# Performance work log

Measured on AMD Instinct MI355X. Metric: run time of the kernel, lower is better.

## Reference

```python
import jax, jax.numpy as jnp
import numpy as np

B, LQ, LK, F = 8, 4096, 4096, 64


def setup_inputs() -> dict:
    key = jax.random.key(0)
    ks = jax.random.split(key, 9)
    s = 1.0 / np.sqrt(F)
    return {
        "query": jax.random.normal(ks[0], (B, LQ, F), dtype=jnp.float32),
        "key": jax.random.normal(ks[1], (B, LK, F), dtype=jnp.float32),
        "value": jax.random.normal(ks[2], (B, LQ, F), dtype=jnp.float32),
        "wq": jax.random.normal(ks[3], (F, F), dtype=jnp.float32) * s,
        "bq": jax.random.normal(ks[4], (F,), dtype=jnp.float32) * 0.01,
        "wk": jax.random.normal(ks[5], (F, F), dtype=jnp.float32) * s,
        "bk": jax.random.normal(ks[6], (F,), dtype=jnp.float32) * 0.01,
        "wv": jax.random.normal(ks[7], (F, F), dtype=jnp.float32) * s,
        "bv": jax.random.normal(ks[8], (F,), dtype=jnp.float32) * 0.01,
    }


def reference(query, key, value, wq, bq, wk, bk, wv, bv):
    # nn.Linear: x @ W.T + b
    q = query @ wq.T + bq          # [B, LQ, F]
    k = key @ wk.T + bk            # [B, LK, F]
    v = value @ wv.T + bv          # [B, LQ, F]
    # scores[b, i, j] = <k_i, q_j>; NO 1/sqrt(d) scaling (faithful to source)
    scores = jnp.einsum('bkf,bqf->bkq', k, q)       # [B, LK, LQ]
    attn = jax.nn.softmax(scores, axis=-1)          # softmax over query positions
    return jnp.einsum('bkq,bqf->bkf', attn, v)      # [B, LK, F]
```

## Files before the change

kernel.cpp:

```cpp
#include <hip/hip_runtime.h>


typedef unsigned short u16;
typedef __attribute__((ext_vector_type(4))) unsigned int u32x4;
typedef __attribute__((ext_vector_type(4))) float f32x4;
typedef __attribute__((ext_vector_type(16))) float f32x16;
typedef __attribute__((ext_vector_type(2))) float f32x2;
typedef __attribute__((ext_vector_type(8))) short s16x8;

#define MFMA32(a, bb, c) __builtin_amdgcn_mfma_f32_32x32x16_bf16((a), (bb), (c), 0, 0, 0)
#define MFMA16(a, bb, c) __builtin_amdgcn_mfma_f32_16x16x32_bf16((a), (bb), (c), 0, 0, 0)

#if __has_builtin(__builtin_amdgcn_exp2f)
#define FEXP2(x) __builtin_amdgcn_exp2f(x)
#else
#define FEXP2(x) exp2f(x)
#endif

__device__ __forceinline__ short f2bf(float x) {
    unsigned u = __builtin_bit_cast(unsigned, x);
    u += 0x7fffu + ((u >> 16) & 1u);
    return (short)(u >> 16);
}
__device__ __forceinline__ float bf2f(short h) {
    unsigned u = ((unsigned)(u16)h) << 16;
    return __builtin_bit_cast(float, u);
}
__device__ __forceinline__ f32x4 zero4() { f32x4 r = {0.f, 0.f, 0.f, 0.f}; return r; }

__device__ __forceinline__ unsigned pktrunc(float lo, float hi) {
#if __has_builtin(__builtin_amdgcn_perm)
    return __builtin_amdgcn_perm(__builtin_bit_cast(unsigned, hi),
                                 __builtin_bit_cast(unsigned, lo), 0x07060302u);
#else
    return (__builtin_bit_cast(unsigned, hi) & 0xffff0000u)
         | (__builtin_bit_cast(unsigned, lo) >> 16);
#endif
}

__device__ __forceinline__ void split8(f32x4 a, f32x4 b, s16x8& hi, s16x8& lo) {
#pragma unroll
    for (int i = 0; i < 4; i++) {
        short h = f2bf(a[i]);
        hi[i] = h;
        lo[i] = f2bf(a[i] - bf2f(h));
    }
#pragma unroll
    for (int i = 0; i < 4; i++) {
        short h = f2bf(b[i]);
        hi[i + 4] = h;
        lo[i + 4] = f2bf(b[i] - bf2f(h));
    }
}

__global__ __launch_bounds__(256) void proj_qkv_32727650796335(
    const float* __restrict__ q_, const float* __restrict__ k_, const float* __restrict__ v_,
    const float* __restrict__ wq, const float* __restrict__ bq,
    const float* __restrict__ wk, const float* __restrict__ bk,
    const float* __restrict__ wv, const float* __restrict__ bv,
    u16* __restrict__ qp, u16* __restrict__ kph, u16* __restrict__ kpl,
    u16* __restrict__ vp) {
    const int z = blockIdx.y;
    const float* X  = (z == 0) ? q_ : (z == 1) ? k_ : v_;
    const float* W  = (z == 0) ? wq : (z == 1) ? wk : wv;
    const float* bi = (z == 0) ? bq : (z == 1) ? bk : bv;

    const int t = threadIdx.x;
    const int w = t >> 6, ln = t & 63, g = ln >> 4, lq = ln & 15;
    const int cidx = blockIdx.x;

    __shared__ f32x4 ldsX[1024];
    __shared__ __align__(16) u16 outH[4096];
    __shared__ __align__(16) u16 outLo[4096];

    const f32x4* X4 = (const f32x4*)X + (size_t)cidx * 1024;
#pragma unroll
    for (int kk = 0; kk < 4; kk++) {
        int lin = t + 256 * kk;
        int r = lin >> 4, c4 = lin & 15;
        ldsX[r * 16 + (c4 ^ (r & 7))] = X4[lin];
    }
    __syncthreads();

    float bv4[4];
#pragma unroll
    for (int nt = 0; nt < 4; nt++) bv4[nt] = bi[lq + 16 * nt];

    const f32x4* W4 = (const f32x4*)W;
    s16x8 wfh[4][2], wfl[4][2];
#pragma unroll
    for (int nt = 0; nt < 4; nt++)
#pragma unroll
        for (int kb = 0; kb < 2; kb++) {
            f32x4 a = W4[(lq + 16 * nt) * 16 + (g + 8 * kb)];
            f32x4 b = W4[(lq + 16 * nt) * 16 + (g + 4 + 8 * kb)];
            split8(a, b, wfh[nt][kb], wfl[nt][kb]);
        }

    s16x8 afh[2], afl[2];
#pragma unroll
    for (int kb = 0; kb < 2; kb++) {
        f32x4 a = ldsX[(16 * w + lq) * 16 + ((g + 8 * kb) ^ (lq & 7))];
        f32x4 b = ldsX[(16 * w + lq) * 16 + ((g + 4 + 8 * kb) ^ (lq & 7))];
        split8(a, b, afh[kb], afl[kb]);
    }

    f32x4 acc[4];
#pragma unroll
    for (int nt = 0; nt < 4; nt++) acc[nt] = zero4();
#pragma unroll
    for (int kb = 0; kb < 2; kb++)
#pragma unroll
        for (int nt = 0; nt < 4; nt++) {
            acc[nt] = MFMA16(afh[kb], wfh[nt][kb], acc[nt]);
            acc[nt] = MFMA16(afh[kb], wfl[nt][kb], acc[nt]);
            acc[nt] = MFMA16(afl[kb], wfh[nt][kb], acc[nt]);
        }

#pragma unroll
    for (int nt = 0; nt < 4; nt++)
#pragma unroll
        for (int r = 0; r < 4; r++) {
            float val = acc[nt][r] + bv4[nt];
            if (z == 1) val *= 1.44269504f;
            short hi = f2bf(val);
            int row = 16 * w + 4 * g + r;
            int f = lq + 16 * nt;
            unsigned idx;
            if (z == 0) {
                idx = (unsigned)((row >> 5) * 2048 + nt * 512
                    + ((row & 31) + ((lq >> 3) & 1) * 32) * 8 + (lq & 7));
            } else if (z == 1) {
                idx = (unsigned)(row * 64 + f);
            } else {
                idx = (unsigned)((f >> 5) * 2048 + (row >> 4) * 512
                    + ((f & 31) + ((row >> 2) & 1) * 32) * 8
                    + ((row >> 3) & 1) * 4 + (row & 3));
            }
            outH[idx] = (u16)hi;
            if (z == 1) outLo[idx] = (u16)f2bf(val - bf2f(hi));
        }
    __syncthreads();

    u16* dH = (z == 0) ? qp : (z == 1) ? kph : vp;
    u32x4* d4 = (u32x4*)(dH + (size_t)cidx * 4096);
    const u32x4* sH = (const u32x4*)outH;
    d4[t] = sH[t];
    d4[t + 256] = sH[t + 256];
    if (z == 1) {
        u32x4* d4l = (u32x4*)(kpl + (size_t)cidx * 4096);
        const u32x4* sL = (const u32x4*)outLo;
        d4l[t] = sL[t];
        d4l[t + 256] = sL[t + 256];
    }
}

__global__ __launch_bounds__(256, 4) void attn_fwd_32727650796335(
    const u16* __restrict__ qp, const u16* __restrict__ kph,
    const u16* __restrict__ kpl, const u16* __restrict__ vp,
    float* __restrict__ out, float* __restrict__ pO, f32x2* __restrict__ pML,
    int nsplit) {
    const int t = threadIdx.x;
    const int w = t >> 6, ln = t & 63, i5 = ln & 31, h = ln >> 5;
    const int itile = blockIdx.x, b = blockIdx.y, split = blockIdx.z;
    const int nc = 64 / nsplit;
    const int c0 = split * nc;

    __shared__ u32x4 ldsbuf[1024];
    const char* ldsc = (const char*)ldsbuf;

    const int irow = b * 4096 + itile * 128 + 32 * w + i5;
    const u16* krh = kph + (size_t)irow * 64;
    const u16* krl = kpl + (size_t)irow * 64;
    s16x8 kfh[4], kfl[4];
#pragma unroll
    for (int ks = 0; ks < 4; ks++) {
        kfh[ks] = *(const s16x8*)(krh + 16 * ks + 8 * h);
        kfl[ks] = *(const s16x8*)(krl + 16 * ks + 8 * h);
    }

    f32x16 oacc0 = {}, oacc1 = {};
    float m = -__builtin_inff();
    float lsum = 0.f;

    const u32x4* qsrc = (const u32x4*)(qp + (size_t)(b * 64) * 4096);
    const u32x4* vsrc = (const u32x4*)(vp + (size_t)(b * 64) * 4096);

    u32x4 qa, qb, va, vb;
#define LOADC(c) do { size_t o_ = (size_t)(c) * 512 + t;      \
        qa = qsrc[o_]; qb = qsrc[o_ + 256];                   \
        va = vsrc[o_]; vb = vsrc[o_ + 256]; } while (0)

    LOADC(c0);
    for (int cc = 0; cc < nc; cc++) {
        __syncthreads();
        ldsbuf[t] = qa;
        ldsbuf[t + 256] = qb;
        ldsbuf[t + 512] = va;
        ldsbuf[t + 768] = vb;
        __syncthreads();
        if (cc + 1 < nc) LOADC(c0 + cc + 1);

        f32x16 s0 = {}, s1 = {};
#pragma unroll
        for (int ks = 0; ks < 4; ks++) {
            const int fo = ks * 1024 + ln * 16;
            s16x8 q0 = *(const s16x8*)(ldsc + fo);
            s16x8 q1 = *(const s16x8*)(ldsc + 4096 + fo);
            s0 = MFMA32(q0, kfh[ks], s0);
            s1 = MFMA32(q1, kfh[ks], s1);
            s0 = MFMA32(q0, kfl[ks], s0);
            s1 = MFMA32(q1, kfl[ks], s1);
        }

        float mx[16];
#pragma unroll
        for (int r = 0; r < 16; r++) mx[r] = fmaxf(s0[r], s1[r]);
#pragma unroll
        for (int st = 8; st > 0; st >>= 1)
#pragma unroll
            for (int r = 0; r < 8; r++)
                if (r < st) mx[r] = fmaxf(mx[r], mx[r + st]);
        float pmax = fmaxf(mx[0], __shfl_xor(mx[0], 32));

        if (!__all(pmax <= m + 8.f)) {
            float mnew = fmaxf(m, pmax);
            float corr = FEXP2(m - mnew);
            lsum *= corr;
#pragma unroll
            for (int r = 0; r < 16; r++) { oacc0[r] *= corr; oacc1[r] *= corr; }
            m = mnew;
        }

        float psum = 0.f;
#pragma unroll
        for (int r = 0; r < 16; r++) {
            s0[r] = FEXP2(s0[r] - m);
            s1[r] = FEXP2(s1[r] - m);
            psum += s0[r] + s1[r];
        }
        psum += __shfl_xor(psum, 32);
        lsum += psum;

        s16x8 pf[4];
#pragma unroll
        for (int qh = 0; qh < 2; qh++) {
            u32x4 pa, pb;
#pragma unroll
            for (int r = 0; r < 4; r++) {
                pa[r] = pktrunc(s0[8 * qh + 2 * r], s0[8 * qh + 2 * r + 1]);
                pb[r] = pktrunc(s1[8 * qh + 2 * r], s1[8 * qh + 2 * r + 1]);
            }
            pf[qh]     = __builtin_bit_cast(s16x8, pa);
            pf[2 + qh] = __builtin_bit_cast(s16x8, pb);
        }

#pragma unroll
        for (int s4 = 0; s4 < 4; s4++) {
            s16x8 vf0 = *(const s16x8*)(ldsc + 8192 + s4 * 1024 + ln * 16);
            s16x8 vf1 = *(const s16x8*)(ldsc + 12288 + s4 * 1024 + ln * 16);
            oacc0 = MFMA32(vf0, pf[s4], oacc0);
            oacc1 = MFMA32(vf1, pf[s4], oacc1);
        }
    }
#undef LOADC

    if (nsplit == 1) {
        float inv = 1.f / lsum;
#pragma unroll
        for (int q = 0; q < 4; q++) {
            f32x4 o0, o1;
#pragma unroll
            for (int r = 0; r < 4; r++) {
                o0[r] = oacc0[4 * q + r] * inv;
                o1[r] = oacc1[4 * q + r] * inv;
            }
            *(f32x4*)(out + (size_t)irow * 64 + 8 * q + 4 * h) = o0;
            *(f32x4*)(out + (size_t)irow * 64 + 32 + 8 * q + 4 * h) = o1;
        }
    } else {
        size_t base = ((size_t)split * 32768 + (size_t)irow) * 64;
#pragma unroll
        for (int q = 0; q < 4; q++) {
            f32x4 o0, o1;
#pragma unroll
            for (int r = 0; r < 4; r++) {
                o0[r] = oacc0[4 * q + r];
                o1[r] = oacc1[4 * q + r];
            }
            *(f32x4*)(pO + base + 8 * q + 4 * h) = o0;
            *(f32x4*)(pO + base + 32 + 8 * q + 4 * h) = o1;
        }
        if (ln < 32) {
            f32x2 ml; ml[0] = m; ml[1] = lsum;
            pML[(size_t)split * 32768 + irow] = ml;
        }
    }
}

__global__ __launch_bounds__(256) void combine_32727650796335(
    const float* __restrict__ pO, const f32x2* __restrict__ pML,
    float* __restrict__ out, int nsplit) {
    const int bt = blockIdx.x;
    const int t = threadIdx.x;
    const int row = t >> 2, fb = (t & 3) << 4;
    const size_t grow = (size_t)bt * 64 + row;

    float M = -__builtin_inff();
#pragma unroll
    for (int s = 0; s < 4; s++)
        if (s < nsplit) M = fmaxf(M, pML[(size_t)s * 32768 + grow][0]);

    float wgt[4];
    float W = 0.f;
#pragma unroll
    for (int s = 0; s < 4; s++) {
        if (s < nsplit) {
            f32x2 ml = pML[(size_t)s * 32768 + grow];
            wgt[s] = exp2f(ml[0] - M);
            W += wgt[s] * ml[1];
        } else wgt[s] = 0.f;
    }
    float inv = 1.f / W;

#pragma unroll
    for (int ff = 0; ff < 16; ff += 4) {
        f32x4 acc = zero4();
#pragma unroll
        for (int s = 0; s < 4; s++)
            if (s < nsplit)
                acc += wgt[s] * *(const f32x4*)(pO + ((size_t)s * 32768 + grow) * 64 + fb + ff);
        *(f32x4*)(out + grow * 64 + fb + ff) = acc * inv;
    }
}

extern "C" void kernel_launch(void* const* d_in, const int* in_sizes, int n_in,
                              void* d_out, int out_size, void* d_ws, size_t ws_size,
                              hipStream_t stream) {
    (void)in_sizes; (void)n_in; (void)out_size;
    const float* q_ = (const float*)d_in[0];
    const float* k_ = (const float*)d_in[1];
    const float* v_ = (const float*)d_in[2];
    const float* wq = (const float*)d_in[3];
    const float* bq = (const float*)d_in[4];
    const float* wk = (const float*)d_in[5];
    const float* bk = (const float*)d_in[6];
    const float* wv = (const float*)d_in[7];
    const float* bv = (const float*)d_in[8];

    const size_t PLANE = (size_t)8 * 4096 * 64;
    u16* qp  = (u16*)d_ws;
    u16* kph = qp + PLANE;
    u16* kpl = kph + PLANE;
    u16* vp  = kpl + PLANE;
    const size_t planes_bytes = 4 * PLANE * sizeof(u16);

    auto fits = [&](int js) {
        size_t need = planes_bytes
                    + (size_t)js * 32768 * 64 * sizeof(float)
                    + (size_t)js * 32768 * sizeof(f32x2);
        return need <= ws_size;
    };
    int nsplit = fits(4) ? 4 : (fits(2) ? 2 : 1);

    float* pO  = (float*)((char*)d_ws + planes_bytes);
    f32x2* pML = (f32x2*)((char*)d_ws + planes_bytes
                          + (size_t)nsplit * 32768 * 64 * sizeof(float));

    proj_qkv_32727650796335<<<dim3(512, 3, 1), 256, 0, stream>>>(
        q_, k_, v_, wq, bq, wk, bk, wv, bv, qp, kph, kpl, vp);
    attn_fwd_32727650796335<<<dim3(32, 8, nsplit), 256, 0, stream>>>(
        qp, kph, kpl, vp, (float*)d_out, pO, pML, nsplit);
    if (nsplit > 1)
        combine_32727650796335<<<dim3(512, 1, 1), 256, 0, stream>>>(
            pO, pML, (float*)d_out, nsplit);
}
```

Measured before the change: 117.3 us.

## Double-buffer Q/V LDS tiles, raise MFMA wave priority, restructure max reduction

Stages Q/V chunks into two alternating LDS buffers so each loop iteration needs one barrier instead of two. The next chunk is written to the spare buffer after the PV MFMAs finish. The MFMA sections are bracketed with s_setprio so waves issuing matrix ops are favoured by the scheduler. The row-max reduction is rewritten as a flatter tree of 3-input max operations. LDS use doubles (32 KB per block), which may cut occupancy from the 4 blocks per CU named in the launch bounds.

```diff
diff --git a/kernel.cpp b/kernel.cpp
--- a/kernel.cpp
+++ b/kernel.cpp
@@ -166,8 +166,7 @@
     const int nc = 64 / nsplit;
     const int c0 = split * nc;
 
-    __shared__ u32x4 ldsbuf[1024];
-    const char* ldsc = (const char*)ldsbuf;
+    __shared__ u32x4 ldsbuf[2][1024];
 
     const int irow = b * 4096 + itile * 128 + 32 * w + i5;
     const u16* krh = kph + (size_t)irow * 64;
@@ -192,16 +191,19 @@
         va = vsrc[o_]; vb = vsrc[o_ + 256]; } while (0)
 
     LOADC(c0);
+    ldsbuf[0][t] = qa;
+    ldsbuf[0][t + 256] = qb;
+    ldsbuf[0][t + 512] = va;
+    ldsbuf[0][t + 768] = vb;
+
+    int cur = 0;
     for (int cc = 0; cc < nc; cc++) {
         __syncthreads();
-        ldsbuf[t] = qa;
-        ldsbuf[t + 256] = qb;
-        ldsbuf[t + 512] = va;
-        ldsbuf[t + 768] = vb;
-        __syncthreads();
         if (cc + 1 < nc) LOADC(c0 + cc + 1);
+        const char* ldsc = (const char*)ldsbuf[cur];
 
         f32x16 s0 = {}, s1 = {};
+        __builtin_amdgcn_s_setprio(1);
 #pragma unroll
         for (int ks = 0; ks < 4; ks++) {
             const int fo = ks * 1024 + ln * 16;
@@ -212,16 +214,22 @@
             s0 = MFMA32(q0, kfl[ks], s0);
             s1 = MFMA32(q1, kfl[ks], s1);
         }
-
-        float mx[16];
-#pragma unroll
-        for (int r = 0; r < 16; r++) mx[r] = fmaxf(s0[r], s1[r]);
-#pragma unroll
-        for (int st = 8; st > 0; st >>= 1)
-#pragma unroll
-            for (int r = 0; r < 8; r++)
-                if (r < st) mx[r] = fmaxf(mx[r], mx[r + st]);
-        float pmax = fmaxf(mx[0], __shfl_xor(mx[0], 32));
+        __builtin_amdgcn_s_setprio(0);
+
+        float mx[11];
+#pragma unroll
+        for (int r = 0; r < 10; r++)
+            mx[r] = fmaxf(fmaxf((r < 8 ? s0[2 * r] : s1[2 * (r - 8)]),
+                                (r < 8 ? s0[2 * r + 1] : s1[2 * (r - 8) + 1])),
+                          (r < 8 ? (r < 5 ? s1[r + 6] : s0[r + 11])
+                                 : s1[2 * (r - 8) + 4]));
+        mx[10] = fmaxf(s1[2], s1[3]);
+        float a0 = fmaxf(fmaxf(mx[0], mx[1]), mx[2]);
+        float a1 = fmaxf(fmaxf(mx[3], mx[4]), mx[5]);
+        float a2 = fmaxf(fmaxf(mx[6], mx[7]), mx[8]);
+        float a3 = fmaxf(mx[9], mx[10]);
+        float pmax = fmaxf(fmaxf(a0, a1), fmaxf(a2, a3));
+        pmax = fmaxf(pmax, __shfl_xor(pmax, 32));
 
         if (!__all(pmax <= m + 8.f)) {
             float mnew = fmaxf(m, pmax);
@@ -255,6 +263,7 @@
             pf[2 + qh] = __builtin_bit_cast(s16x8, pb);
         }
 
+        __builtin_amdgcn_s_setprio(1);
 #pragma unroll
         for (int s4 = 0; s4 < 4; s4++) {
             s16x8 vf0 = *(const s16x8*)(ldsc + 8192 + s4 * 1024 + ln * 16);
@@ -262,6 +271,15 @@
             oacc0 = MFMA32(vf0, pf[s4], oacc0);
             oacc1 = MFMA32(vf1, pf[s4], oacc1);
         }
+        __builtin_amdgcn_s_setprio(0);
+
+        if (cc + 1 < nc) {
+            ldsbuf[cur ^ 1][t] = qa;
+            ldsbuf[cur ^ 1][t + 256] = qb;
+            ldsbuf[cur ^ 1][t + 512] = va;
+            ldsbuf[cur ^ 1][t + 768] = vb;
+        }
+        cur ^= 1;
     }
 #undef LOADC
 
```

New measurement: 112.2 us. -4.3%, faster.
